# Performance work log

Measured on AMD Instinct MI355X. Metric: run time of the kernel, lower is better.

Reference implementation:

```python
import jax, jax.numpy as jnp
import numpy as np

T, D, H = 2048, 1024, 16
HS = D // H  # head_size = 64
DFF = 4 * D
LN_EPS = 1e-6


def layernorm(x, scale, bias, eps=LN_EPS):
    mu = jnp.mean(x, axis=-1, keepdims=True)
    var = jnp.mean(jnp.square(x - mu), axis=-1, keepdims=True)
    return (x - mu) * jax.lax.rsqrt(var + eps) * scale + bias


def setup_inputs() -> dict:
    key = jax.random.key(0)
    ks = jax.random.split(key, 12)
    s_in = 1.0 / np.sqrt(D)
    s_ff = 1.0 / np.sqrt(DFF)
    return {
        "x": jax.random.normal(ks[0], (T, D), jnp.float32),
        "Wq": jax.random.normal(ks[1], (H, D, HS), jnp.float32) * s_in,
        "Wk": jax.random.normal(ks[2], (H, D, HS), jnp.float32) * s_in,
        "Wv": jax.random.normal(ks[3], (H, D, HS), jnp.float32) * s_in,
        "Wo": jax.random.normal(ks[4], (D, D), jnp.float32) * s_in,
        "bo": jnp.zeros((D,), jnp.float32),
        "W1": jax.random.normal(ks[5], (D, DFF), jnp.float32) * s_in,
        "b1": jnp.zeros((DFF,), jnp.float32),
        "W2": jax.random.normal(ks[6], (DFF, D), jnp.float32) * s_ff,
        "b2": jnp.zeros((D,), jnp.float32),
        "ln1_scale": jnp.ones((D,), jnp.float32),
        "ln1_bias": jnp.zeros((D,), jnp.float32),
        "ln2_scale": jnp.ones((D,), jnp.float32),
        "ln2_bias": jnp.zeros((D,), jnp.float32),
        "training": 0,
    }


def reference(x, Wq, Wk, Wv, Wo, bo, W1, b1, W2, b2,
              ln1_scale, ln1_bias, ln2_scale, ln2_bias, training):
    # --- pre-LN causal multi-head self-attention ---
    h = layernorm(x, ln1_scale, ln1_bias)
    q = jnp.einsum("td,hdk->htk", h, Wq)  # [H,T,HS]
    k = jnp.einsum("td,hdk->htk", h, Wk)
    v = jnp.einsum("td,hdk->htk", h, Wv)
    scores = jnp.einsum("htk,hsk->hts", q, k) / jnp.sqrt(jnp.float32(HS))
    causal = jnp.tril(jnp.ones((T, T), jnp.float32))
    scores = jnp.where(causal == 0, -jnp.inf, scores)
    wei = jax.nn.softmax(scores, axis=-1)
    av = jnp.einsum("hts,hsk->htk", wei, v)          # [H,T,HS]
    av = av.transpose(1, 0, 2).reshape(T, H * HS)    # concat over heads
    x = x + av @ Wo + bo                              # dropout deterministic -> identity
    # --- pre-LN feed-forward ---
    h2 = layernorm(x, ln2_scale, ln2_bias)
    ff = jax.nn.relu(h2 @ W1 + b1) @ W2 + b2
    x = x + ff
    return x
```

## Files before the change

kernel.cpp:

```cpp
#include <hip/hip_runtime.h>
#include <cstdint>


typedef __bf16 bf16;
typedef __bf16 bf16x4 __attribute__((ext_vector_type(4)));
typedef __bf16 bf16x8 __attribute__((ext_vector_type(8)));
typedef float floatx4 __attribute__((ext_vector_type(4)));

__device__ __forceinline__ void ld_g2l(const bf16* g, bf16* l) {
    __builtin_amdgcn_global_load_lds(
        (const __attribute__((address_space(1))) void*)g,
        (__attribute__((address_space(3))) void*)l, 16, 0, 0);
}

__device__ __forceinline__ void ln_row_body(
    const float* __restrict__ x, const float* __restrict__ sc,
    const float* __restrict__ bi, bf16* __restrict__ out,
    int row, int tid, float* wred)
{
    const float4 v = ((const float4*)(x + (size_t)row * 1024))[tid];
    float s1 = v.x + v.y + v.z + v.w;
    float s2 = v.x * v.x + v.y * v.y + v.z * v.z + v.w * v.w;
#pragma unroll
    for (int mm = 1; mm < 64; mm <<= 1) {
        s1 += __shfl_xor(s1, mm);
        s2 += __shfl_xor(s2, mm);
    }
    const int wave = tid >> 6, lane = tid & 63;
    if (lane == 0) { wred[wave] = s1; wred[4 + wave] = s2; }
    __syncthreads();
    s1 = wred[0] + wred[1] + wred[2] + wred[3];
    s2 = wred[4] + wred[5] + wred[6] + wred[7];
    const float mu = s1 * (1.f / 1024.f);
    const float var = fmaxf(s2 * (1.f / 1024.f) - mu * mu, 0.f);
    const float rr = rsqrtf(var + 1e-6f);
    const float4 scv = ((const float4*)sc)[tid];
    const float4 biv = ((const float4*)bi)[tid];
    bf16x4 ov;
    ov[0] = (bf16)((v.x - mu) * rr * scv.x + biv.x);
    ov[1] = (bf16)((v.y - mu) * rr * scv.y + biv.y);
    ov[2] = (bf16)((v.z - mu) * rr * scv.z + biv.z);
    ov[3] = (bf16)((v.w - mu) * rr * scv.w + biv.w);
    *(bf16x4*)(out + (size_t)row * 1024 + tid * 4) = ov;
}

__global__ __launch_bounds__(256) void prep_kernel(
    const float* __restrict__ Wq, const float* __restrict__ Wk,
    const float* __restrict__ Wv, bf16* __restrict__ Wqkvt,
    const float* __restrict__ x, const float* __restrict__ ln1s,
    const float* __restrict__ ln1b, bf16* __restrict__ hbuf)
{
    __shared__ float tile[64][65];
    __shared__ float wred[8];
    const int b = blockIdx.x;
    const int tid = threadIdx.x;

    if (b >= 768) {
        ln_row_body(x, ln1s, ln1b, hbuf, b - 768, tid, wred);
        return;
    }

    const int tx = tid & 63, ty = tid >> 6;
    const int sec = b >> 4, ti = b & 15;
    const int m = sec >> 4, h = sec & 15;
    const float* src = (m == 0 ? Wq : (m == 1 ? Wk : Wv)) + h * 65536;
    bf16* dst = Wqkvt + m * 1048576 + h * 65536;
    const int r0 = ti * 64;
#pragma unroll
    for (int i = ty; i < 64; i += 4)
        tile[i][tx] = src[(size_t)(r0 + i) * 64 + tx];
    __syncthreads();
#pragma unroll
    for (int i = ty; i < 64; i += 4)
        dst[(size_t)i * 1024 + r0 + tx] = (bf16)tile[tx][i];
}

__global__ __launch_bounds__(256) void ln_kernel(
    const float* __restrict__ x, const float* __restrict__ sc,
    const float* __restrict__ bi, bf16* __restrict__ out)
{
    __shared__ float wred[8];
    ln_row_body(x, sc, bi, out, blockIdx.x, threadIdx.x, wred);
}

__global__ __launch_bounds__(256) void reduce4_kernel(
    const bf16* __restrict__ p, const float* __restrict__ bias,
    const float* __restrict__ res, float* __restrict__ out)
{
    const int idx = blockIdx.x * 256 + threadIdx.x;
    const size_t e = (size_t)idx * 8;
    const int c = (int)(e & 1023);
    const bf16x8 a0 = *(const bf16x8*)(p + e);
    const bf16x8 a1 = *(const bf16x8*)(p + 2097152 + e);
    const bf16x8 a2 = *(const bf16x8*)(p + 4194304 + e);
    const bf16x8 a3 = *(const bf16x8*)(p + 6291456 + e);
    const float4 b0 = *(const float4*)(bias + c);
    const float4 b1 = *(const float4*)(bias + c + 4);
    const float4 r0 = *(const float4*)(res + e);
    const float4 r1 = *(const float4*)(res + e + 4);
    float o[8];
#pragma unroll
    for (int i = 0; i < 8; ++i)
        o[i] = ((float)a0[i] + (float)a1[i]) + ((float)a2[i] + (float)a3[i]);
    float4 o0, o1;
    o0.x = o[0] + b0.x + r0.x; o0.y = o[1] + b0.y + r0.y;
    o0.z = o[2] + b0.z + r0.z; o0.w = o[3] + b0.w + r0.w;
    o1.x = o[4] + b1.x + r1.x; o1.y = o[5] + b1.y + r1.y;
    o1.z = o[6] + b1.z + r1.z; o1.w = o[7] + b1.w + r1.w;
    *(float4*)(out + e) = o0;
    *(float4*)(out + e + 4) = o1;
}

template <int MODE, int NG, int MG, int SPLITK>
__global__ __launch_bounds__(512) void gemm128_kernel(
    const bf16* __restrict__ A, const bf16* __restrict__ Bt,
    int N, int K,
    float* __restrict__ outF, bf16* __restrict__ outB,
    const float* __restrict__ bias)
{
    __shared__ __align__(16) bf16 Alds[2][128][64];
    __shared__ __align__(16) bf16 Blds[2][128][64];
    const int tid  = threadIdx.x;
    const int lane = tid & 63;
    const int w    = tid >> 6;
    const int r15  = lane & 15;
    const int quad = lane >> 4;

    const int id    = blockIdx.x + gridDim.x * (blockIdx.y + gridDim.y * blockIdx.z);
    const int xcd   = id & 7;
    const int seq   = id >> 3;
    const int nPerX = gridDim.x / NG;
    const int mPerX = gridDim.y / MG;
    const int nm    = nPerX * mPerX;
    const int z     = seq / nm;
    const int loc   = seq - z * nm;
    const int bn    = ((xcd % NG) * nPerX + (loc % nPerX)) * 128;
    const int bm    = ((xcd / NG) * mPerX + (loc / nPerX)) * 128;

    const int wm = (w >> 2) * 64;
    const int wn = (w & 3) * 32;

    floatx4 acc[4][2];
#pragma unroll
    for (int i = 0; i < 4; ++i)
#pragma unroll
        for (int j = 0; j < 2; ++j) acc[i][j] = (floatx4)(0.f);

    const int KS    = K / SPLITK;
    const int kBase = (SPLITK > 1) ? z * KS : 0;
    const int nIter = KS / 64;

    const int lrow = lane >> 3;
    const int gch  = (lane & 7) ^ lrow;
    const bf16* aptr = A + (size_t)(bm + w * 16 + lrow) * K + kBase + gch * 8;
    const bf16* bptr = Bt + (size_t)(bn + w * 16 + lrow) * K + kBase + gch * 8;

#pragma unroll
    for (int t = 0; t < 2; ++t) {
        ld_g2l(aptr + (size_t)(t * 8) * K, &Alds[0][w * 16 + t * 8][0]);
        ld_g2l(bptr + (size_t)(t * 8) * K, &Blds[0][w * 16 + t * 8][0]);
    }

    for (int it = 0; it < nIter; ++it) {
        const int buf = it & 1;
        __syncthreads();
        if (it + 1 < nIter) {
            const int k2 = (it + 1) * 64;
#pragma unroll
            for (int t = 0; t < 2; ++t) {
                ld_g2l(aptr + (size_t)(t * 8) * K + k2, &Alds[buf ^ 1][w * 16 + t * 8][0]);
                ld_g2l(bptr + (size_t)(t * 8) * K + k2, &Blds[buf ^ 1][w * 16 + t * 8][0]);
            }
        }
#pragma unroll
        for (int kk = 0; kk < 2; ++kk) {
            const int pc = ((kk * 4 + quad) ^ (r15 & 7)) * 8;
            bf16x8 af[4], bfr[2];
#pragma unroll
            for (int i = 0; i < 4; ++i)
                af[i] = *(const bf16x8*)(&Alds[buf][wm + i * 16 + r15][pc]);
#pragma unroll
            for (int j = 0; j < 2; ++j)
                bfr[j] = *(const bf16x8*)(&Blds[buf][wn + j * 16 + r15][pc]);
#pragma unroll
            for (int i = 0; i < 4; ++i)
#pragma unroll
                for (int j = 0; j < 2; ++j)
                    acc[i][j] = __builtin_amdgcn_mfma_f32_16x16x32_bf16(
                        af[i], bfr[j], acc[i][j], 0, 0, 0);
        }
    }

    const int row0 = bm + wm + quad * 4;
    const int col0 = bn + wn + r15;

    if (MODE == 1 && bn >= 2048) {
        bf16* vt = (bf16*)outF;
#pragma unroll
        for (int i = 0; i < 4; ++i) {
            const int row = row0 + i * 16;
#pragma unroll
            for (int j = 0; j < 2; ++j) {
                const int col = col0 + j * 16 - 2048;
                bf16x4 pv;
#pragma unroll
                for (int reg = 0; reg < 4; ++reg) pv[reg] = (bf16)acc[i][j][reg];
                *(bf16x4*)(vt + (size_t)(col >> 6) * 131072
                              + (size_t)(col & 63) * 2048 + row) = pv;
            }
        }
        return;
    }

    bf16* po = (MODE == 3) ? outB + (size_t)z * 2097152 : outB;
#pragma unroll
    for (int i = 0; i < 4; ++i) {
#pragma unroll
        for (int reg = 0; reg < 4; ++reg) {
            const int row = row0 + i * 16 + reg;
#pragma unroll
            for (int j = 0; j < 2; ++j) {
                const int col = col0 + j * 16;
                float v = acc[i][j][reg];
                if (MODE == 0 || MODE == 1) {
                    outB[(size_t)row * N + col] = (bf16)v;
                } else if (MODE == 2) {
                    v += bias[col];
                    outB[(size_t)row * N + col] = (bf16)fmaxf(v, 0.f);
                } else {
                    po[(size_t)row * N + col] = (bf16)v;
                }
            }
        }
    }
}

template <int NG, int MG>
__global__ __launch_bounds__(256) void oproj_kernel(
    const bf16* __restrict__ Opart, const float* __restrict__ Lpart,
    const bf16* __restrict__ Bt,
    float* __restrict__ outF, const float* __restrict__ bias,
    const float* __restrict__ res)
{
    const int N = 1024, K = 1024;
    __shared__ __align__(16) bf16 Alds[2][64][64];
    __shared__ __align__(16) bf16 Blds[2][64][64];
    const int tid  = threadIdx.x;
    const int lane = tid & 63;
    const int w    = tid >> 6;
    const int r15  = lane & 15;
    const int quad = lane >> 4;

    const int id    = blockIdx.x + gridDim.x * blockIdx.y;
    const int xcd   = id & 7;
    const int seq   = id >> 3;
    const int nPerX = gridDim.x / NG;
    const int mPerX = gridDim.y / MG;
    const int loc   = seq % (nPerX * mPerX);
    const int bn    = ((xcd % NG) * nPerX + (loc % nPerX)) * 64;
    const int bm    = ((xcd / NG) * mPerX + (loc / nPerX)) * 64;

    const int wm = (w >> 1) * 32;
    const int wn = (w & 1) * 32;
    const int qt = bm >> 6;
    const bool hasB = (qt > 0);

    floatx4 acc[2][2];
#pragma unroll
    for (int i = 0; i < 2; ++i)
#pragma unroll
        for (int j = 0; j < 2; ++j) acc[i][j] = (floatx4)(0.f);

    const int nIter = K / 64;
    const int lrow = lane >> 3;
    const int gch  = (lane & 7) ^ lrow;
    const bf16* bptr = Bt + (size_t)(bn + w * 16 + lrow) * K + gch * 8;

    const int rit0 = w * 16 + lrow;
    const int rit1 = rit0 + 8;

#pragma unroll
    for (int t = 0; t < 2; ++t)
        ld_g2l(bptr + (size_t)(t * 8) * K, &Blds[0][w * 16 + t * 8][0]);
    {
        const size_t tb = (size_t)qt * 4096;
#pragma unroll
        for (int t = 0; t < 2; ++t) {
            const int rit = t ? rit1 : rit0;
            const size_t off = tb + (size_t)rit * 64 + gch * 8;
            const bf16x8 a = *(const bf16x8*)(Opart + off);
            float la = Lpart[qt * 64 + rit];
            bf16x8 bv; float lb = 0.f;
#pragma unroll
            for (int i = 0; i < 8; ++i) bv[i] = (bf16)0.f;
            if (hasB) {
                bv = *(const bf16x8*)(Opart + 2097152 + off);
                lb = Lpart[32768 + qt * 64 + rit];
            }
            const float inv = 1.f / (la + lb);
            bf16x8 o;
#pragma unroll
            for (int i = 0; i < 8; ++i)
                o[i] = (bf16)(((float)a[i] + (float)bv[i]) * inv);
            *(bf16x8*)(&Alds[0][w * 16 + t * 8 + lrow][(lane & 7) * 8]) = o;
        }
    }

    for (int it = 0; it < nIter; ++it) {
        const int buf = it & 1;
        __syncthreads();
        bf16x8 na[2], nb[2];
        float nla[2], nlb[2];
        const bool pf = (it + 1 < nIter);
        if (pf) {
            const int k2 = (it + 1) * 64;
#pragma unroll
            for (int t = 0; t < 2; ++t)
                ld_g2l(bptr + (size_t)(t * 8) * K + k2, &Blds[buf ^ 1][w * 16 + t * 8][0]);
            const size_t tb = (size_t)((it + 1) * 32 + qt) * 4096;
#pragma unroll
            for (int t = 0; t < 2; ++t) {
                const int rit = t ? rit1 : rit0;
                const size_t off = tb + (size_t)rit * 64 + gch * 8;
                na[t] = *(const bf16x8*)(Opart + off);
                nla[t] = Lpart[((it + 1) * 32 + qt) * 64 + rit];
#pragma unroll
                for (int i = 0; i < 8; ++i) nb[t][i] = (bf16)0.f;
                nlb[t] = 0.f;
                if (hasB) {
                    nb[t] = *(const bf16x8*)(Opart + 2097152 + off);
                    nlb[t] = Lpart[32768 + ((it + 1) * 32 + qt) * 64 + rit];
                }
            }
        }
#pragma unroll
        for (int kk = 0; kk < 2; ++kk) {
            const int pc = ((kk * 4 + quad) ^ (r15 & 7)) * 8;
            bf16x8 af[2], bfr[2];
#pragma unroll
            for (int i = 0; i < 2; ++i)
                af[i] = *(const bf16x8*)(&Alds[buf][wm + i * 16 + r15][pc]);
#pragma unroll
            for (int j = 0; j < 2; ++j)
                bfr[j] = *(const bf16x8*)(&Blds[buf][wn + j * 16 + r15][pc]);
#pragma unroll
            for (int i = 0; i < 2; ++i)
#pragma unroll
                for (int j = 0; j < 2; ++j)
                    acc[i][j] = __builtin_amdgcn_mfma_f32_16x16x32_bf16(
                        af[i], bfr[j], acc[i][j], 0, 0, 0);
        }
        if (pf) {
#pragma unroll
            for (int t = 0; t < 2; ++t) {
                const float inv = 1.f / (nla[t] + nlb[t]);
                bf16x8 o;
#pragma unroll
                for (int i = 0; i < 8; ++i)
                    o[i] = (bf16)(((float)na[t][i] + (float)nb[t][i]) * inv);
                *(bf16x8*)(&Alds[buf ^ 1][w * 16 + t * 8 + lrow][(lane & 7) * 8]) = o;
            }
        }
    }

    const int row0 = bm + wm + quad * 4;
    const int col0 = bn + wn + r15;
#pragma unroll
    for (int i = 0; i < 2; ++i)
#pragma unroll
        for (int reg = 0; reg < 4; ++reg) {
            const int row = row0 + i * 16 + reg;
#pragma unroll
            for (int j = 0; j < 2; ++j) {
                const int col = col0 + j * 16;
                outF[(size_t)row * N + col] =
                    acc[i][j][reg] + bias[col] + res[(size_t)row * N + col];
            }
        }
}

__global__ __launch_bounds__(256) void attn_kernel(
    const bf16* __restrict__ qkv, const bf16* __restrict__ vt,
    bf16* __restrict__ Opart, float* __restrict__ Lpart,
    const float* __restrict__ Wo, bf16* __restrict__ Wot,
    const float* __restrict__ W1, bf16* __restrict__ W1t,
    const float* __restrict__ W2, bf16* __restrict__ W2t)
{
    __shared__ __align__(16) union SM {
        struct {
            bf16 PQ[4096];
            bf16 Ks[2][64][64];
            bf16 Vs[2][64][64];
        } a;
        float tile[64][65];
    } sm;

    const int tid  = threadIdx.x;
    const int b    = blockIdx.x;

    if (b >= 1024) {
        const int i = b - 1024;
        const float* src; bf16* dst; int R, C, c0, r0;
        if (i < 256) {
            src = Wo; dst = Wot; R = 1024; C = 1024;
            c0 = (i & 15) * 64; r0 = (i >> 4) * 64;
        } else if (i < 1280) {
            const int j = i - 256;
            src = W1; dst = W1t; R = 1024; C = 4096;
            c0 = (j & 63) * 64; r0 = (j >> 6) * 64;
        } else {
            const int j = i - 1280;
            src = W2; dst = W2t; R = 4096; C = 1024;
            c0 = (j & 15) * 64; r0 = (j >> 4) * 64;
        }
        const int tx = tid & 63, ty = tid >> 6;
#pragma unroll
        for (int k = ty; k < 64; k += 4)
            sm.tile[k][tx] = src[(size_t)(r0 + k) * C + c0 + tx];
        __syncthreads();
#pragma unroll
        for (int k = ty; k < 64; k += 4)
            dst[(size_t)(c0 + k) * R + r0 + tx] = (bf16)sm.tile[tx][k];
        return;
    }

    const int w    = tid >> 6;
    const int lane = tid & 63;
    const int r15  = lane & 15;
    const int quad = lane >> 4;
    const int rl   = lane >> 3;
    const int gsw  = (lane & 7) ^ (rl & 7);

    const int idp  = b & 255;
    const int seq  = idp >> 3;
    const int h    = (idp & 7) * 2 + (seq & 1);
    const int qp   = seq >> 1;
    const int qt   = ((b >> 8) & 1) ? 31 - qp : qp;
    const int half = b >> 9;
    const int qrow0 = qt * 64;

    const int n0    = (qt + 2) >> 1;
    const int sbBeg = half ? n0 : 0;
    const int sbEnd = half ? qt + 1 : n0;

    if (sbBeg >= sbEnd) return;

    const int tile = half * 512 + h * 32 + qt;
    const size_t obase = (size_t)tile * 4096;

    const bf16* qsec = qkv + h * 64;
    const bf16* ksec = qkv + 1024 + h * 64;
    const bf16* vth  = vt + (size_t)h * 64 * 2048;
    const int s0 = sbBeg * 64;

#pragma unroll
    for (int t = 0; t < 2; ++t) {
        const int r = t * 32 + w * 8 + rl;
        ld_g2l(qsec + (size_t)(qrow0 + r) * 3072 + gsw * 8, &sm.a.PQ[(t * 32 + w * 8) * 64]);
        ld_g2l(ksec + (size_t)(s0 + r) * 3072 + gsw * 8, &sm.a.Ks[0][t * 32 + w * 8][0]);
        ld_g2l(vth + (size_t)r * 2048 + s0 + gsw * 8, &sm.a.Vs[0][t * 32 + w * 8][0]);
    }
    __syncthreads();

    bf16x8 qf[2];
#pragma unroll
    for (int c = 0; c < 2; ++c) {
        const int p = ((c * 4 + quad) ^ (r15 & 7)) * 8;
        qf[c] = *(const bf16x8*)&sm.a.PQ[(w * 16 + r15) * 64 + p];
    }

    float lacc[4] = {0.f, 0.f, 0.f, 0.f};
    floatx4 O[4];
#pragma unroll
    for (int j = 0; j < 4; ++j) O[j] = (floatx4)(0.f);

    int ns = 0;
#pragma unroll 1
    for (int sb = sbBeg; sb < sbEnd; ++sb, ++ns) {
        const int buf = ns & 1;
        if (sb + 1 < sbEnd) {
            const int s1 = (sb + 1) * 64;
#pragma unroll
            for (int t = 0; t < 2; ++t) {
                const int r = t * 32 + w * 8 + rl;
                ld_g2l(ksec + (size_t)(s1 + r) * 3072 + gsw * 8, &sm.a.Ks[buf ^ 1][t * 32 + w * 8][0]);
                ld_g2l(vth + (size_t)r * 2048 + s1 + gsw * 8, &sm.a.Vs[buf ^ 1][t * 32 + w * 8][0]);
            }
        }

        floatx4 S[4];
#pragma unroll
        for (int j = 0; j < 4; ++j) S[j] = (floatx4)(0.f);
        __builtin_amdgcn_s_setprio(1);
#pragma unroll
        for (int c = 0; c < 2; ++c) {
#pragma unroll
            for (int j = 0; j < 4; ++j) {
                const int p = ((c * 4 + quad) ^ (r15 & 7)) * 8;
                const bf16x8 kb = *(const bf16x8*)&sm.a.Ks[buf][j * 16 + r15][p];
                S[j] = __builtin_amdgcn_mfma_f32_16x16x32_bf16(qf[c], kb, S[j], 0, 0, 0);
            }
        }
        __builtin_amdgcn_s_setprio(0);
        if (sb == qt) {
            const int rowl = w * 16 + quad * 4;
#pragma unroll
            for (int j = 0; j < 4; ++j) {
                const int col = j * 16 + r15;
#pragma unroll
                for (int r = 0; r < 4; ++r) {
                    float p = exp2f(fmaf(S[j][r], 0.18033688f, -28.853901f));
                    if (col > rowl + r) p = 0.f;
                    S[j][r] = p;
                    lacc[r] += p;
                }
            }
        } else {
#pragma unroll
            for (int j = 0; j < 4; ++j)
#pragma unroll
                for (int r = 0; r < 4; ++r) {
                    const float p = exp2f(fmaf(S[j][r], 0.18033688f, -28.853901f));
                    S[j][r] = p;
                    lacc[r] += p;
                }
        }
#pragma unroll
        for (int r = 0; r < 4; ++r) {
            const int prow = quad * 4 + r;
            const int swz = (prow & 7) << 3;
#pragma unroll
            for (int j = 0; j < 4; ++j)
                sm.a.PQ[w * 1024 + prow * 64 + ((j * 16 + r15) ^ swz)] = (bf16)S[j][r];
        }
        __builtin_amdgcn_s_setprio(1);
#pragma unroll
        for (int c = 0; c < 2; ++c) {
            const bf16x8 a = *(const bf16x8*)&sm.a.PQ[
                w * 1024 + r15 * 64 + ((c * 32 + quad * 8) ^ ((r15 & 7) << 3))];
#pragma unroll
            for (int j = 0; j < 4; ++j) {
                const int p = ((c * 4 + quad) ^ (r15 & 7)) * 8;
                const bf16x8 vb = *(const bf16x8*)&sm.a.Vs[buf][j * 16 + r15][p];
                O[j] = __builtin_amdgcn_mfma_f32_16x16x32_bf16(a, vb, O[j], 0, 0, 0);
            }
        }
        __builtin_amdgcn_s_setprio(0);
        __syncthreads();
    }
#pragma unroll
    for (int r = 0; r < 4; ++r) {
#pragma unroll
        for (int d = 1; d < 16; d <<= 1) lacc[r] += __shfl_xor(lacc[r], d);
    }
#pragma unroll
    for (int r = 0; r < 4; ++r) {
        const int row = w * 16 + quad * 4 + r;
#pragma unroll
        for (int j = 0; j < 4; ++j)
            Opart[obase + (size_t)row * 64 + j * 16 + r15] = (bf16)(O[j][r]);
    }
    if (r15 == 0) {
#pragma unroll
        for (int r = 0; r < 4; ++r)
            Lpart[tile * 64 + w * 16 + quad * 4 + r] = lacc[r];
    }
}

extern "C" void kernel_launch(void* const* d_in, const int* in_sizes, int n_in,
                              void* d_out, int out_size, void* d_ws, size_t ws_size,
                              hipStream_t stream)
{
    const float* x    = (const float*)d_in[0];
    const float* Wq   = (const float*)d_in[1];
    const float* Wk   = (const float*)d_in[2];
    const float* Wv   = (const float*)d_in[3];
    const float* Wo   = (const float*)d_in[4];
    const float* bo   = (const float*)d_in[5];
    const float* W1   = (const float*)d_in[6];
    const float* b1   = (const float*)d_in[7];
    const float* W2   = (const float*)d_in[8];
    const float* b2   = (const float*)d_in[9];
    const float* ln1s = (const float*)d_in[10];
    const float* ln1b = (const float*)d_in[11];
    const float* ln2s = (const float*)d_in[12];
    const float* ln2b = (const float*)d_in[13];

    char* ws = (char*)d_ws;
    bf16*  Wqkvt = (bf16*)(ws + 0);
    bf16*  Wot   = (bf16*)(ws + 6291456);
    bf16*  W1t   = (bf16*)(ws + 8388608);
    bf16*  W2t   = (bf16*)(ws + 16777216);
    bf16*  hbuf  = (bf16*)(ws + 25165824);
    bf16*  QKV   = (bf16*)(ws + 29360128);
    bf16*  Vt    = (bf16*)(ws + 41943040);
    float* x1    = (float*)(ws + 50331648);
    bf16*  h2    = (bf16*)(ws + 58720256);
    bf16*  ff1   = (bf16*)(ws + 62914560);
    bf16*  psum  = (bf16*)(ws + 79691776);
    bf16*  Opart = (bf16*)(ws + 79691776);
    float* Lpart = (float*)(ws + 96468992);

    prep_kernel<<<2816, 256, 0, stream>>>(Wq, Wk, Wv, Wqkvt, x, ln1s, ln1b, hbuf);
    gemm128_kernel<1,4,2,1><<<dim3(24, 16), 512, 0, stream>>>(hbuf, Wqkvt, 3072, 1024, (float*)Vt, QKV, nullptr);
    attn_kernel<<<3328, 256, 0, stream>>>(QKV, Vt, Opart, Lpart,
                                          Wo, Wot, W1, W1t, W2, W2t);
    oproj_kernel<4,2><<<dim3(16, 32), 256, 0, stream>>>(Opart, Lpart, Wot, x1, bo, x);
    ln_kernel<<<2048, 256, 0, stream>>>(x1, ln2s, ln2b, h2);
    gemm128_kernel<2,4,2,1><<<dim3(32, 16), 512, 0, stream>>>(h2, W1t, 4096, 1024, nullptr, ff1, b1);
    gemm128_kernel<3,2,4,4><<<dim3(8, 16, 4), 512, 0, stream>>>(ff1, W2t, 1024, 4096, nullptr, psum, nullptr);
    reduce4_kernel<<<1024, 256, 0, stream>>>(psum, b2, x1, (float*)d_out);
}
```

Measured before the change: 236.1 us.

## Prefetch K/V two blocks ahead through registers instead of direct global-to-LDS loads

The attention loop now loads K and V tiles from global memory into registers two blocks ahead, then writes them into the alternate LDS buffer at the end of each step. This replaces the async global_load_lds double buffer. The loop is manually unrolled twice so the two register sets can alternate. The aim is to hide global load latency behind a full iteration of MFMA and softmax work. The cost is higher register pressure, an extra LDS write per step, and explicit lgkmcnt waits plus a barrier.

```diff
diff --git a/kernel.cpp b/kernel.cpp
--- a/kernel.cpp
+++ b/kernel.cpp
@@ -430,6 +430,7 @@
     const int quad = lane >> 4;
     const int rl   = lane >> 3;
     const int gsw  = (lane & 7) ^ (rl & 7);
+    const int wch  = (lane & 7) * 8;
 
     const int idp  = b & 255;
     const int seq  = idp >> 3;
@@ -452,6 +453,7 @@
     const bf16* ksec = qkv + 1024 + h * 64;
     const bf16* vth  = vt + (size_t)h * 64 * 2048;
     const int s0 = sbBeg * 64;
+    const int wr = w * 8 + rl;
 
 #pragma unroll
     for (int t = 0; t < 2; ++t) {
@@ -462,6 +464,15 @@
     }
     __syncthreads();
 
+    bf16x8 kA0, kA1, vA0, vA1, kB0, kB1, vB0, vB1;
+    {
+        const int s1 = (sbBeg + 1 < sbEnd ? sbBeg + 1 : sbEnd - 1) * 64;
+        kA0 = *(const bf16x8*)(ksec + (size_t)(s1 + wr) * 3072 + gsw * 8);
+        kA1 = *(const bf16x8*)(ksec + (size_t)(s1 + 32 + wr) * 3072 + gsw * 8);
+        vA0 = *(const bf16x8*)(vth + (size_t)wr * 2048 + s1 + gsw * 8);
+        vA1 = *(const bf16x8*)(vth + (size_t)(32 + wr) * 2048 + s1 + gsw * 8);
+    }
+
     bf16x8 qf[2];
 #pragma unroll
     for (int c = 0; c < 2; ++c) {
@@ -474,80 +485,95 @@
 #pragma unroll
     for (int j = 0; j < 4; ++j) O[j] = (floatx4)(0.f);
 
-    int ns = 0;
-#pragma unroll 1
-    for (int sb = sbBeg; sb < sbEnd; ++sb, ++ns) {
-        const int buf = ns & 1;
-        if (sb + 1 < sbEnd) {
-            const int s1 = (sb + 1) * 64;
-#pragma unroll
-            for (int t = 0; t < 2; ++t) {
-                const int r = t * 32 + w * 8 + rl;
-                ld_g2l(ksec + (size_t)(s1 + r) * 3072 + gsw * 8, &sm.a.Ks[buf ^ 1][t * 32 + w * 8][0]);
-                ld_g2l(vth + (size_t)r * 2048 + s1 + gsw * 8, &sm.a.Vs[buf ^ 1][t * 32 + w * 8][0]);
-            }
-        }
-
-        floatx4 S[4];
-#pragma unroll
-        for (int j = 0; j < 4; ++j) S[j] = (floatx4)(0.f);
-        __builtin_amdgcn_s_setprio(1);
-#pragma unroll
-        for (int c = 0; c < 2; ++c) {
-#pragma unroll
-            for (int j = 0; j < 4; ++j) {
-                const int p = ((c * 4 + quad) ^ (r15 & 7)) * 8;
-                const bf16x8 kb = *(const bf16x8*)&sm.a.Ks[buf][j * 16 + r15][p];
-                S[j] = __builtin_amdgcn_mfma_f32_16x16x32_bf16(qf[c], kb, S[j], 0, 0, 0);
-            }
-        }
-        __builtin_amdgcn_s_setprio(0);
-        if (sb == qt) {
-            const int rowl = w * 16 + quad * 4;
-#pragma unroll
-            for (int j = 0; j < 4; ++j) {
-                const int col = j * 16 + r15;
-#pragma unroll
-                for (int r = 0; r < 4; ++r) {
-                    float p = exp2f(fmaf(S[j][r], 0.18033688f, -28.853901f));
-                    if (col > rowl + r) p = 0.f;
-                    S[j][r] = p;
-                    lacc[r] += p;
-                }
-            }
-        } else {
-#pragma unroll
-            for (int j = 0; j < 4; ++j)
-#pragma unroll
-                for (int r = 0; r < 4; ++r) {
-                    const float p = exp2f(fmaf(S[j][r], 0.18033688f, -28.853901f));
-                    S[j][r] = p;
-                    lacc[r] += p;
-                }
-        }
-#pragma unroll
-        for (int r = 0; r < 4; ++r) {
-            const int prow = quad * 4 + r;
-            const int swz = (prow & 7) << 3;
-#pragma unroll
-            for (int j = 0; j < 4; ++j)
-                sm.a.PQ[w * 1024 + prow * 64 + ((j * 16 + r15) ^ swz)] = (bf16)S[j][r];
-        }
-        __builtin_amdgcn_s_setprio(1);
-#pragma unroll
-        for (int c = 0; c < 2; ++c) {
-            const bf16x8 a = *(const bf16x8*)&sm.a.PQ[
-                w * 1024 + r15 * 64 + ((c * 32 + quad * 8) ^ ((r15 & 7) << 3))];
-#pragma unroll
-            for (int j = 0; j < 4; ++j) {
-                const int p = ((c * 4 + quad) ^ (r15 & 7)) * 8;
-                const bf16x8 vb = *(const bf16x8*)&sm.a.Vs[buf][j * 16 + r15][p];
-                O[j] = __builtin_amdgcn_mfma_f32_16x16x32_bf16(a, vb, O[j], 0, 0, 0);
-            }
-        }
-        __builtin_amdgcn_s_setprio(0);
-        __syncthreads();
-    }
+#define ATTN_STEP(CK0, CK1, CV0, CV1, NK0, NK1, NV0, NV1)                      \
+    {                                                                          \
+              \
+        const int sld = (sb + 2 < sbEnd ? sb + 2 : sbEnd - 1) * 64;            \
+        NK0 = *(const bf16x8*)(ksec + (size_t)(sld + wr) * 3072 + gsw * 8);    \
+        NK1 = *(const bf16x8*)(ksec + (size_t)(sld + 32 + wr) * 3072 + gsw * 8);\
+        NV0 = *(const bf16x8*)(vth + (size_t)wr * 2048 + sld + gsw * 8);       \
+        NV1 = *(const bf16x8*)(vth + (size_t)(32 + wr) * 2048 + sld + gsw * 8);\
+        floatx4 S[4];                                                          \
+        _Pragma("unroll")                                                      \
+        for (int j = 0; j < 4; ++j) S[j] = (floatx4)(0.f);                     \
+        __builtin_amdgcn_s_setprio(1);                                         \
+        _Pragma("unroll")                                                      \
+        for (int c = 0; c < 2; ++c) {                                          \
+            _Pragma("unroll")                                                  \
+            for (int j = 0; j < 4; ++j) {                                      \
+                const int p = ((c * 4 + quad) ^ (r15 & 7)) * 8;                \
+                const bf16x8 kb = *(const bf16x8*)&sm.a.Ks[bufc][j * 16 + r15][p];\
+                S[j] = __builtin_amdgcn_mfma_f32_16x16x32_bf16(qf[c], kb, S[j], 0, 0, 0);\
+            }                                                                  \
+        }                                                                      \
+        __builtin_amdgcn_s_setprio(0);                                         \
+        if (sb == qt) {                                                        \
+            const int rowl = w * 16 + quad * 4;                                \
+            _Pragma("unroll")                                                  \
+            for (int j = 0; j < 4; ++j) {                                      \
+                const int col = j * 16 + r15;                                  \
+                _Pragma("unroll")                                              \
+                for (int r = 0; r < 4; ++r) {                                  \
+                    float pv = exp2f(fmaf(S[j][r], 0.18033688f, -28.853901f)); \
+                    if (col > rowl + r) pv = 0.f;                              \
+                    S[j][r] = pv;                                              \
+                    lacc[r] += pv;                                             \
+                }                                                              \
+            }                                                                  \
+        } else {                                                               \
+            _Pragma("unroll")                                                  \
+            for (int j = 0; j < 4; ++j)                                        \
+                _Pragma("unroll")                                              \
+                for (int r = 0; r < 4; ++r) {                                  \
+                    const float pv = exp2f(fmaf(S[j][r], 0.18033688f, -28.853901f));\
+                    S[j][r] = pv;                                              \
+                    lacc[r] += pv;                                             \
+                }                                                              \
+        }                                                                      \
+        _Pragma("unroll")                                                      \
+        for (int r = 0; r < 4; ++r) {                                          \
+            const int prow = quad * 4 + r;                                     \
+            const int swz = (prow & 7) << 3;                                   \
+            _Pragma("unroll")                                                  \
+            for (int j = 0; j < 4; ++j)                                        \
+                sm.a.PQ[w * 1024 + prow * 64 + ((j * 16 + r15) ^ swz)] = (bf16)S[j][r];\
+        }                                                                      \
+        __builtin_amdgcn_s_setprio(1);                                         \
+        _Pragma("unroll")                                                      \
+        for (int c = 0; c < 2; ++c) {                                          \
+            const bf16x8 a = *(const bf16x8*)&sm.a.PQ[                         \
+                w * 1024 + r15 * 64 + ((c * 32 + quad * 8) ^ ((r15 & 7) << 3))];\
+            _Pragma("unroll")                                                  \
+            for (int j = 0; j < 4; ++j) {                                      \
+                const int p = ((c * 4 + quad) ^ (r15 & 7)) * 8;                \
+                const bf16x8 vb = *(const bf16x8*)&sm.a.Vs[bufc][j * 16 + r15][p];\
+                O[j] = __builtin_amdgcn_mfma_f32_16x16x32_bf16(a, vb, O[j], 0, 0, 0);\
+            }                                                                  \
+        }                                                                      \
+        __builtin_amdgcn_s_setprio(0);                                         \
+                        \
+        if (sb + 1 < sbEnd) {                                                  \
+            const int nb_ = bufc ^ 1;                                          \
+            *(bf16x8*)&sm.a.Ks[nb_][wr][wch]      = CK0;                       \
+            *(bf16x8*)&sm.a.Ks[nb_][32 + wr][wch] = CK1;                       \
+            *(bf16x8*)&sm.a.Vs[nb_][wr][wch]      = CV0;                       \
+            *(bf16x8*)&sm.a.Vs[nb_][32 + wr][wch] = CV1;                       \
+        }                                                                      \
+        asm volatile("s_waitcnt lgkmcnt(0)" ::: "memory");                     \
+        __builtin_amdgcn_s_barrier();                                          \
+    }
+
+    int sb = sbBeg, bufc = 0;
+    while (true) {
+        ATTN_STEP(kA0, kA1, vA0, vA1, kB0, kB1, vB0, vB1);
+        ++sb; bufc ^= 1;
+        if (sb >= sbEnd) break;
+        ATTN_STEP(kB0, kB1, vB0, vB1, kA0, kA1, vA0, vA1);
+        ++sb; bufc ^= 1;
+        if (sb >= sbEnd) break;
+    }
+#undef ATTN_STEP
+
 #pragma unroll
     for (int r = 0; r < 4; ++r) {
 #pragma unroll
```

Result: slower. 241.1 us (+2.1%).
